# Kernel tuning notes

Measured on AMD Instinct MI355X. Metric: run time of the kernel, lower is better.

Reference implementation:

```python
import jax, jax.numpy as jnp
import numpy as np


def setup_inputs() -> dict:
    key = jax.random.key(0)
    kq, kk, kv = jax.random.split(key, 3)
    B, H, S, D = 4, 16, 2048, 64
    q = jax.random.normal(kq, (B, H, S, D), dtype=jnp.float32)
    k = jax.random.normal(kk, (B, H, S, D), dtype=jnp.float32)
    v = jax.random.normal(kv, (B, H, S, D), dtype=jnp.float32)
    return {"q": q, "k": k, "v": v}


def reference(q, k, v):
    # Flash-attention math (causal=True, softmax_scale = 1/sqrt(head_dim)).
    D = q.shape[-1]
    scale = 1.0 / np.sqrt(D).astype(np.float32)
    # scores: [B, H, Sq, Sk]
    scores = jnp.einsum('bhqd,bhkd->bhqk', q, k) * scale
    Sq, Sk = scores.shape[-2], scores.shape[-1]
    causal_mask = jnp.tril(jnp.ones((Sq, Sk), dtype=bool))  # [Sq, Sk]
    neg_inf = jnp.asarray(jnp.finfo(scores.dtype).min, scores.dtype)
    scores = jnp.where(causal_mask, scores, neg_inf)
    probs = jax.nn.softmax(scores, axis=-1)
    out = jnp.einsum('bhqk,bhkd->bhqd', probs, v)
    return out
```

## Files before the change

kernel.cpp:

```cpp
#include <hip/hip_runtime.h>
#include <hip/hip_bf16.h>

#define S_LEN 2048
#define DH 64
#define QBLK 128
#define KVBLK 64
#define LDPK 72
#define LDPV 68

typedef __attribute__((ext_vector_type(4))) float f32x4;
typedef __attribute__((ext_vector_type(8))) short short8v;
typedef __attribute__((ext_vector_type(4))) unsigned uint4v;
typedef __attribute__((ext_vector_type(2))) unsigned uint2v;

__device__ __forceinline__ unsigned cvt_pk(float a, float b) {
    unsigned r;
    asm("v_cvt_pk_bf16_f32 %0, %1, %2" : "=v"(r) : "v"(a), "v"(b));
    return r;
}

__global__ __launch_bounds__(512) void fa_fwd_kernel(
    const float* __restrict__ Q, const float* __restrict__ K,
    const float* __restrict__ V, float* __restrict__ O)
{
    const int tid  = threadIdx.x;
    const int lane = tid & 63;
    const int w    = tid >> 6;
    const int bh   = blockIdx.x & 63;
    const int p    = blockIdx.x >> 6;

    const size_t base = (size_t)bh * S_LEN * DH;
    const float* Qg = Q + base;
    const float* Kg = K + base;
    const float* Vg = V + base;
    float*       Og = O + base;

    __shared__ __align__(16) short K_lds[KVBLK][LDPK];
    __shared__ __align__(16) short V_lds[DH][LDPV];

    const int lr = lane & 15;
    const int lg = lane >> 4;

    const int kr = tid >> 3;
    const int dc = (tid & 7) * 8;
    const int vd = tid & 63;
    const int vg = tid >> 6;

    unsigned kpfu[4], vpf[4];

    auto prefetch = [&](int kvb) {
        const float* kp = Kg + (size_t)(kvb + kr) * DH + dc;
        f32x4 a = *(const f32x4*)kp;
        f32x4 b = *(const f32x4*)(kp + 4);
        kpfu[0] = cvt_pk(a[0], a[1]);
        kpfu[1] = cvt_pk(a[2], a[3]);
        kpfu[2] = cvt_pk(b[0], b[1]);
        kpfu[3] = cvt_pk(b[2], b[3]);
        #pragma unroll
        for (int i = 0; i < 4; ++i) {
            int kv = vg * 8 + i * 2;
            float x = Vg[(size_t)(kvb + kv) * DH + vd];
            float y = Vg[(size_t)(kvb + kv + 1) * DH + vd];
            vpf[i] = cvt_pk(x, y);
        }
    };

    auto stage = [&]() {
        uint4v u = {kpfu[0], kpfu[1], kpfu[2], kpfu[3]};
        *(uint4v*)&K_lds[kr][dc] = u;
        #pragma unroll
        for (int i = 0; i < 4; ++i) {
            int kv = vg * 8 + i * 2;
            *(unsigned*)((char*)&V_lds[0][0] + vd * (LDPV * 2) + kv * 2) = vpf[i];
        }
    };

    const float qscale = 0.125f * 1.44269504088896340736f;

    prefetch(0);

    #pragma unroll 1
    for (int t = 0; t < 2; ++t) {
        const int qb = (t == 0) ? (15 - p) : p;
        const int q0 = qb * QBLK + w * 16;
        const int kv_end = (qb + 1) * QBLK;

        short8v qfrag[2];
        #pragma unroll
        for (int kf = 0; kf < 2; ++kf) {
            const float* qp = Qg + (size_t)(q0 + lr) * DH + kf * 32 + lg * 8;
            f32x4 a = *(const f32x4*)qp;
            f32x4 b = *(const f32x4*)(qp + 4);
            uint4v u;
            u[0] = cvt_pk(a[0] * qscale, a[1] * qscale);
            u[1] = cvt_pk(a[2] * qscale, a[3] * qscale);
            u[2] = cvt_pk(b[0] * qscale, b[1] * qscale);
            u[3] = cvt_pk(b[2] * qscale, b[3] * qscale);
            qfrag[kf] = __builtin_bit_cast(short8v, u);
        }

        f32x4 o_acc[4];
        #pragma unroll
        for (int i = 0; i < 4; ++i)
            o_acc[i] = (f32x4){0.f, 0.f, 0.f, 0.f};
        float m_run = -1e30f, l_run = 0.f;

        for (int kvb = 0; kvb < kv_end; kvb += KVBLK) {
            __syncthreads();
            stage();
            __syncthreads();

            int nxt = kvb + KVBLK;
            if (nxt < kv_end)  prefetch(nxt);
            else if (t == 0)   prefetch(0);

            if (kvb <= q0 + 15) {
                f32x4 s_acc[4];
                #pragma unroll
                for (int kt = 0; kt < 4; ++kt)
                    s_acc[kt] = (f32x4){0.f, 0.f, 0.f, 0.f};

                __builtin_amdgcn_s_setprio(1);
                #pragma unroll
                for (int kt = 0; kt < 4; ++kt) {
                    short8v kf0 = *(const short8v*)&K_lds[kt * 16 + lr][lg * 8];
                    short8v kf1 = *(const short8v*)&K_lds[kt * 16 + lr][32 + lg * 8];
                    s_acc[kt] = __builtin_amdgcn_mfma_f32_16x16x32_bf16(
                        kf0, qfrag[0], s_acc[kt], 0, 0, 0);
                    s_acc[kt] = __builtin_amdgcn_mfma_f32_16x16x32_bf16(
                        kf1, qfrag[1], s_acc[kt], 0, 0, 0);
                }
                __builtin_amdgcn_s_setprio(0);

                const int qrow = q0 + lr;
                if (kvb + KVBLK - 1 > q0) {
                    #pragma unroll
                    for (int kt = 0; kt < 4; ++kt)
                        #pragma unroll
                        for (int r = 0; r < 4; ++r) {
                            int kvv = kvb + kt * 16 + lg * 4 + r;
                            if (kvv > qrow) s_acc[kt][r] = -1e30f;
                        }
                }
                float tmax = -1e30f;
                #pragma unroll
                for (int kt = 0; kt < 4; ++kt)
                    #pragma unroll
                    for (int r = 0; r < 4; ++r)
                        tmax = fmaxf(tmax, s_acc[kt][r]);
                tmax = fmaxf(tmax, __shfl_xor(tmax, 16));
                tmax = fmaxf(tmax, __shfl_xor(tmax, 32));
                float mnew = fmaxf(m_run, tmax);
                float corr = __builtin_amdgcn_exp2f(m_run - mnew);
                m_run = mnew;
                float rsum = 0.f;
                #pragma unroll
                for (int kt = 0; kt < 4; ++kt)
                    #pragma unroll
                    for (int r = 0; r < 4; ++r) {
                        float pe = __builtin_amdgcn_exp2f(s_acc[kt][r] - mnew);
                        s_acc[kt][r] = pe;
                        rsum += pe;
                    }
                rsum += __shfl_xor(rsum, 16);
                rsum += __shfl_xor(rsum, 32);
                l_run = l_run * corr + rsum;

                short8v pa[2];
                #pragma unroll
                for (int kf = 0; kf < 2; ++kf) {
                    uint4v u;
                    u[0] = cvt_pk(s_acc[2 * kf][0],     s_acc[2 * kf][1]);
                    u[1] = cvt_pk(s_acc[2 * kf][2],     s_acc[2 * kf][3]);
                    u[2] = cvt_pk(s_acc[2 * kf + 1][0], s_acc[2 * kf + 1][1]);
                    u[3] = cvt_pk(s_acc[2 * kf + 1][2], s_acc[2 * kf + 1][3]);
                    pa[kf] = __builtin_bit_cast(short8v, u);
                }

                #pragma unroll
                for (int r = 0; r < 4; ++r) {
                    float c = __shfl(corr, 4 * lg + r);
                    #pragma unroll
                    for (int dt = 0; dt < 4; ++dt)
                        o_acc[dt][r] *= c;
                }

                __builtin_amdgcn_s_setprio(1);
                #pragma unroll
                for (int dt = 0; dt < 4; ++dt) {
                    const char* vrow = (const char*)&V_lds[0][0] + (dt * 16 + lr) * (LDPV * 2);
                    #pragma unroll
                    for (int kf = 0; kf < 2; ++kf) {
                        uint2v lo = *(const uint2v*)(vrow + (kf * 32 + 4 * lg) * 2);
                        uint2v hi = *(const uint2v*)(vrow + (kf * 32 + 16 + 4 * lg) * 2);
                        uint4v u = {lo[0], lo[1], hi[0], hi[1]};
                        short8v vv = __builtin_bit_cast(short8v, u);
                        o_acc[dt] = __builtin_amdgcn_mfma_f32_16x16x32_bf16(
                            pa[kf], vv, o_acc[dt], 0, 0, 0);
                    }
                }
                __builtin_amdgcn_s_setprio(0);
            }
        }

        float lsum = __shfl(l_run, 4 * lg + ((lane >> 4) & 0));
        #pragma unroll
        for (int r = 0; r < 4; ++r) {
            float ls = __shfl(l_run, 4 * lg + r);
            float inv = 1.0f / ls;
            int qrow = q0 + lg * 4 + r;
            float* op = Og + (size_t)qrow * DH + lr;
            #pragma unroll
            for (int dt = 0; dt < 4; ++dt)
                op[dt * 16] = o_acc[dt][r] * inv;
        }
        (void)lsum;
    }
}

extern "C" void kernel_launch(void* const* d_in, const int* in_sizes, int n_in,
                              void* d_out, int out_size, void* d_ws, size_t ws_size,
                              hipStream_t stream) {
    const float* q = (const float*)d_in[0];
    const float* k = (const float*)d_in[1];
    const float* v = (const float*)d_in[2];
    float* out = (float*)d_out;
    fa_fwd_kernel<<<dim3(512), dim3(512), 0, stream>>>(q, k, v, out);
}
```

Baseline: 79.48 us.

## Double-buffer K/V in LDS and skip softmax rescale when max is stable

Splits the K/V LDS tiles into two buffers so the next tile is staged into the spare buffer after compute, cutting one of the two barriers per KV iteration. Adds a lazy-rescale rule: the running max and output correction are only updated when some row's tile max exceeds the running max by more than 8 (log2 units), which skips the exp and multiply work on most tiles. It also tightens the causal skip condition from kvb <= q0+15 to kvb <= q0. The lazy threshold lets exponent values reach up to 2^8 before rescaling, which trades a little precision headroom for fewer corrections, and the extra buffer doubles LDS use.

```diff
diff --git a/kernel.cpp b/kernel.cpp
--- a/kernel.cpp
+++ b/kernel.cpp
@@ -35,12 +35,11 @@
     const float* Vg = V + base;
     float*       Og = O + base;
 
-    __shared__ __align__(16) short K_lds[KVBLK][LDPK];
-    __shared__ __align__(16) short V_lds[DH][LDPV];
+    __shared__ __align__(16) short K_lds[2][KVBLK][LDPK];
+    __shared__ __align__(16) short V_lds[2][DH][LDPV];
 
     const int lr = lane & 15;
     const int lg = lane >> 4;
-
     const int kr = tid >> 3;
     const int dc = (tid & 7) * 8;
     const int vd = tid & 63;
@@ -65,19 +64,22 @@
         }
     };
 
-    auto stage = [&]() {
+    auto stage = [&](int b) {
         uint4v u = {kpfu[0], kpfu[1], kpfu[2], kpfu[3]};
-        *(uint4v*)&K_lds[kr][dc] = u;
+        *(uint4v*)&K_lds[b][kr][dc] = u;
         #pragma unroll
         for (int i = 0; i < 4; ++i) {
             int kv = vg * 8 + i * 2;
-            *(unsigned*)((char*)&V_lds[0][0] + vd * (LDPV * 2) + kv * 2) = vpf[i];
+            *(unsigned*)((char*)&V_lds[b][0][0] + vd * (LDPV * 2) + kv * 2) = vpf[i];
         }
     };
 
     const float qscale = 0.125f * 1.44269504088896340736f;
 
     prefetch(0);
+    stage(0);
+    int cur = 0;
+    __syncthreads();
 
     #pragma unroll 1
     for (int t = 0; t < 2; ++t) {
@@ -105,16 +107,17 @@
             o_acc[i] = (f32x4){0.f, 0.f, 0.f, 0.f};
         float m_run = -1e30f, l_run = 0.f;
 
+        #pragma unroll 1
         for (int kvb = 0; kvb < kv_end; kvb += KVBLK) {
-            __syncthreads();
-            stage();
-            __syncthreads();
-
-            int nxt = kvb + KVBLK;
-            if (nxt < kv_end)  prefetch(nxt);
-            else if (t == 0)   prefetch(0);
-
-            if (kvb <= q0 + 15) {
+            int nkv = kvb + KVBLK;
+            bool have = true;
+            if (nkv >= kv_end) { if (t == 0) nkv = 0; else have = false; }
+            if (have) prefetch(nkv);
+
+            if (kvb <= q0) {
+                const short (*Kc)[LDPK] = K_lds[cur];
+                const char* Vc = (const char*)&V_lds[cur][0][0];
+
                 f32x4 s_acc[4];
                 #pragma unroll
                 for (int kt = 0; kt < 4; ++kt)
@@ -123,8 +126,8 @@
                 __builtin_amdgcn_s_setprio(1);
                 #pragma unroll
                 for (int kt = 0; kt < 4; ++kt) {
-                    short8v kf0 = *(const short8v*)&K_lds[kt * 16 + lr][lg * 8];
-                    short8v kf1 = *(const short8v*)&K_lds[kt * 16 + lr][32 + lg * 8];
+                    short8v kf0 = *(const short8v*)&Kc[kt * 16 + lr][lg * 8];
+                    short8v kf1 = *(const short8v*)&Kc[kt * 16 + lr][32 + lg * 8];
                     s_acc[kt] = __builtin_amdgcn_mfma_f32_16x16x32_bf16(
                         kf0, qfrag[0], s_acc[kt], 0, 0, 0);
                     s_acc[kt] = __builtin_amdgcn_mfma_f32_16x16x32_bf16(
@@ -142,6 +145,7 @@
                             if (kvv > qrow) s_acc[kt][r] = -1e30f;
                         }
                 }
+
                 float tmax = -1e30f;
                 #pragma unroll
                 for (int kt = 0; kt < 4; ++kt)
@@ -150,21 +154,33 @@
                         tmax = fmaxf(tmax, s_acc[kt][r]);
                 tmax = fmaxf(tmax, __shfl_xor(tmax, 16));
                 tmax = fmaxf(tmax, __shfl_xor(tmax, 32));
-                float mnew = fmaxf(m_run, tmax);
-                float corr = __builtin_amdgcn_exp2f(m_run - mnew);
-                m_run = mnew;
+
+                if (!__all(tmax <= m_run + 8.0f)) {
+                    float mnew = fmaxf(m_run, tmax);
+                    float corr = __builtin_amdgcn_exp2f(m_run - mnew);
+                    m_run = mnew;
+                    l_run *= corr;
+                    #pragma unroll
+                    for (int r = 0; r < 4; ++r) {
+                        float c = __shfl(corr, 4 * lg + r);
+                        #pragma unroll
+                        for (int dt = 0; dt < 4; ++dt)
+                            o_acc[dt][r] *= c;
+                    }
+                }
+
                 float rsum = 0.f;
                 #pragma unroll
                 for (int kt = 0; kt < 4; ++kt)
                     #pragma unroll
                     for (int r = 0; r < 4; ++r) {
-                        float pe = __builtin_amdgcn_exp2f(s_acc[kt][r] - mnew);
+                        float pe = __builtin_amdgcn_exp2f(s_acc[kt][r] - m_run);
                         s_acc[kt][r] = pe;
                         rsum += pe;
                     }
                 rsum += __shfl_xor(rsum, 16);
                 rsum += __shfl_xor(rsum, 32);
-                l_run = l_run * corr + rsum;
+                l_run += rsum;
 
                 short8v pa[2];
                 #pragma unroll
@@ -177,18 +193,10 @@
                     pa[kf] = __builtin_bit_cast(short8v, u);
                 }
 
-                #pragma unroll
-                for (int r = 0; r < 4; ++r) {
-                    float c = __shfl(corr, 4 * lg + r);
-                    #pragma unroll
-                    for (int dt = 0; dt < 4; ++dt)
-                        o_acc[dt][r] *= c;
-                }
-
                 __builtin_amdgcn_s_setprio(1);
                 #pragma unroll
                 for (int dt = 0; dt < 4; ++dt) {
-                    const char* vrow = (const char*)&V_lds[0][0] + (dt * 16 + lr) * (LDPV * 2);
+                    const char* vrow = Vc + (dt * 16 + lr) * (LDPV * 2);
                     #pragma unroll
                     for (int kf = 0; kf < 2; ++kf) {
                         uint2v lo = *(const uint2v*)(vrow + (kf * 32 + 4 * lg) * 2);
@@ -201,9 +209,14 @@
                 }
                 __builtin_amdgcn_s_setprio(0);
             }
-        }
-
-        float lsum = __shfl(l_run, 4 * lg + ((lane >> 4) & 0));
+
+            if (have) {
+                stage(cur ^ 1);
+                __syncthreads();
+            }
+            cur ^= 1;
+        }
+
         #pragma unroll
         for (int r = 0; r < 4; ++r) {
             float ls = __shfl(l_run, 4 * lg + r);
@@ -214,7 +227,6 @@
             for (int dt = 0; dt < 4; ++dt)
                 op[dt * 16] = o_acc[dt][r] * inv;
         }
-        (void)lsum;
     }
 }
 
```

New measurement: 79.02 us. About the same (-0.6%).
